# Kernel optimization log

Measured on AMD Instinct MI355X. Metric: run time of the kernel, lower is better.

## Reference

```python
import jax, jax.numpy as jnp
import numpy as np

H = 768
NHEADS = 2
MAX_REL = 96  # module's max_rel_enc; static here (positive count >> 96 for these inputs)


def _ln(x, g, b, eps=1e-5):
    m = jnp.mean(x, axis=-1, keepdims=True)
    v = jnp.var(x, axis=-1, keepdims=True)
    return (x - m) * jax.lax.rsqrt(v + eps) * g + b


def _mha(q, k, v, in_w, in_b, out_w, out_b, key_pad):
    # q [B,Lq,H], k/v [B,Lk,H], key_pad [B,Lk] bool (True = masked key)
    d = q.shape[-1]
    dh = d // NHEADS
    wq, wk, wv = jnp.split(in_w, 3, axis=0)
    bq, bk, bv = jnp.split(in_b, 3)
    qh = (q @ wq.T + bq).reshape(q.shape[0], q.shape[1], NHEADS, dh)
    kh = (k @ wk.T + bk).reshape(k.shape[0], k.shape[1], NHEADS, dh)
    vh = (v @ wv.T + bv).reshape(v.shape[0], v.shape[1], NHEADS, dh)
    scores = jnp.einsum('bqhd,bkhd->bhqk', qh, kh) / np.float32(np.sqrt(dh))
    scores = jnp.where(key_pad[:, None, None, :], jnp.float32(-1e9), scores)
    attn = jax.nn.softmax(scores, axis=-1)
    out = jnp.einsum('bhqk,bkhd->bqhd', attn, vh).reshape(q.shape)
    return out @ out_w.T + out_b


def _forward(hidden_states, logits_prev, block_mask, W_rel, b_rel,
             enc_in_w, enc_in_b, enc_out_w, enc_out_b,
             enc_l1_w, enc_l1_b, enc_l2_w, enc_l2_b,
             enc_ln1_g, enc_ln1_b, enc_ln2_g, enc_ln2_b,
             dec_in_w, dec_in_b, dec_out_w, dec_out_b,
             dec_l1_w, dec_l1_b, dec_l2_w, dec_l2_b,
             dec_ln1_g, dec_ln1_b, dec_ln2_g, dec_ln2_b,
             fc_w, fc_b):
    B, N, Hd = hidden_states.shape
    # rel_layer(cat([h_i, h_j])) == h_i @ Wa.T + h_j @ Wb.T + b  (avoids [B,N,N,2H] intermediate)
    Wa = W_rel[:, :Hd]
    Wb = W_rel[:, Hd:]
    A = hidden_states @ Wa.T   # [B,N,H]
    C = hidden_states @ Wb.T   # [B,N,H]
    feat_pair = (A[:, :, None, :] + C[:, None, :, :] + b_rel).reshape(B, N * N, Hd)

    bm = block_mask.astype(jnp.float32)
    pair_mask = (bm[:, :, None] * bm[:, None, :]).reshape(B, N * N)
    score = jax.nn.sigmoid(logits_prev).reshape(B, N * N)
    neg = (score < 0.5).astype(jnp.float32)
    neg = 1.0 - (1.0 - neg) * pair_mask           # 1 = negative-or-invalid pair
    neg = jax.lax.stop_gradient(neg)              # matches score_prev.detach_()

    # dynamic top-k gather of positive pairs (static MAX_REL here)
    idx = jnp.argsort(neg, axis=1)[:, :MAX_REL]                     # positives (neg==0) first
    enc_pad = jnp.take_along_axis(neg, idx, axis=1) > 0.5           # [B,MAX_REL]
    enc_pad = enc_pad.at[:, 0].set(False)
    feat_now = feat_pair * (1.0 - neg)[:, :, None]
    pos_pairs = jnp.take_along_axis(feat_now, idx[:, :, None], axis=1)  # [B,MAX_REL,H]

    # 1-layer transformer encoder (post-norm, ReLU, d_ff = H)
    x = pos_pairs
    x = _ln(x + _mha(x, x, x, enc_in_w, enc_in_b, enc_out_w, enc_out_b, enc_pad),
            enc_ln1_g, enc_ln1_b)
    ff = jax.nn.relu(x @ enc_l1_w.T + enc_l1_b) @ enc_l2_w.T + enc_l2_b
    patterns = _ln(x + ff, enc_ln2_g, enc_ln2_b)

    # 1-layer decoder with self_attn=False: cross-attn + FFN, post-norm
    t = feat_pair
    t = _ln(t + _mha(t, patterns, patterns, dec_in_w, dec_in_b, dec_out_w, dec_out_b, enc_pad),
            dec_ln1_g, dec_ln1_b)
    ff = jax.nn.relu(t @ dec_l1_w.T + dec_l1_b) @ dec_l2_w.T + dec_l2_b
    t = _ln(t + ff, dec_ln2_g, dec_ln2_b)

    refined = t.reshape(B, N, N, Hd)
    return (refined @ fc_w.T + fc_b)[..., 0]    # [B,N,N]


def setup_inputs() -> dict:
    key = jax.random.key(0)
    ks = jax.random.split(key, 24)
    B, N = 4, 128
    p = lambda k, s: jax.random.normal(k, s, jnp.float32) * 0.02
    return {
        'hidden_states': jax.random.normal(ks[0], (B, N, H), jnp.float32),
        'logits_prev': jax.random.normal(ks[1], (B, N, N), jnp.float32),
        'block_mask': jax.random.randint(ks[2], (B, N), 0, 2),
        'W_rel': p(ks[3], (H, 2 * H)), 'b_rel': p(ks[4], (H,)),
        'enc_in_w': p(ks[5], (3 * H, H)), 'enc_in_b': p(ks[6], (3 * H,)),
        'enc_out_w': p(ks[7], (H, H)), 'enc_out_b': p(ks[8], (H,)),
        'enc_l1_w': p(ks[9], (H, H)), 'enc_l1_b': p(ks[10], (H,)),
        'enc_l2_w': p(ks[11], (H, H)), 'enc_l2_b': p(ks[12], (H,)),
        'enc_ln1_g': jnp.ones((H,), jnp.float32), 'enc_ln1_b': jnp.zeros((H,), jnp.float32),
        'enc_ln2_g': jnp.ones((H,), jnp.float32), 'enc_ln2_b': jnp.zeros((H,), jnp.float32),
        'dec_in_w': p(ks[13], (3 * H, H)), 'dec_in_b': p(ks[14], (3 * H,)),
        'dec_out_w': p(ks[15], (H, H)), 'dec_out_b': p(ks[16], (H,)),
        'dec_l1_w': p(ks[17], (H, H)), 'dec_l1_b': p(ks[18], (H,)),
        'dec_l2_w': p(ks[19], (H, H)), 'dec_l2_b': p(ks[20], (H,)),
        'dec_ln1_g': jnp.ones((H,), jnp.float32), 'dec_ln1_b': jnp.zeros((H,), jnp.float32),
        'dec_ln2_g': jnp.ones((H,), jnp.float32), 'dec_ln2_b': jnp.zeros((H,), jnp.float32),
        'fc_w': p(ks[21], (1, H)), 'fc_b': p(ks[22], (1,)),
    }


def reference(hidden_states, logits_prev, block_mask, W_rel, b_rel,
              enc_in_w, enc_in_b, enc_out_w, enc_out_b,
              enc_l1_w, enc_l1_b, enc_l2_w, enc_l2_b,
              enc_ln1_g, enc_ln1_b, enc_ln2_g, enc_ln2_b,
              dec_in_w, dec_in_b, dec_out_w, dec_out_b,
              dec_l1_w, dec_l1_b, dec_l2_w, dec_l2_b,
              dec_ln1_g, dec_ln1_b, dec_ln2_g, dec_ln2_b,
              fc_w, fc_b):
    return _forward(hidden_states, logits_prev, block_mask, W_rel, b_rel,
                    enc_in_w, enc_in_b, enc_out_w, enc_out_b,
                    enc_l1_w, enc_l1_b, enc_l2_w, enc_l2_b,
                    enc_ln1_g, enc_ln1_b, enc_ln2_g, enc_ln2_b,
                    dec_in_w, dec_in_b, dec_out_w, dec_out_b,
                    dec_l1_w, dec_l1_b, dec_l2_w, dec_l2_b,
                    dec_ln1_g, dec_ln1_b, dec_ln2_g, dec_ln2_b,
                    fc_w, fc_b)
```

## Files before the change

### kernel.cpp

```cpp
#include <hip/hip_runtime.h>
#include <cstdint>
#include <cstddef>

typedef unsigned short u16;
typedef __attribute__((ext_vector_type(8))) short sv8;
typedef __attribute__((ext_vector_type(4))) short sv4;
typedef __attribute__((ext_vector_type(4))) float fv4;
typedef __attribute__((ext_vector_type(8))) __bf16 bv8;

#define WAITVM(N) asm volatile("s_waitcnt vmcnt(" #N ")" ::: "memory")
#define WAITLG0() asm volatile("s_waitcnt lgkmcnt(0)" ::: "memory")
#define SB0() __builtin_amdgcn_sched_barrier(0)
#define BAR() __builtin_amdgcn_s_barrier()

__device__ __forceinline__ float b2f(u16 u) {
  union { unsigned int i; float f; } v; v.i = ((unsigned int)u) << 16; return v.f;
}
__device__ __forceinline__ u16 f2b(float f) {
  union { float f; unsigned int i; } v; v.f = f;
  unsigned int r = v.i + 0x7fffu + ((v.i >> 16) & 1u);
  return (u16)(r >> 16);
}

__device__ __forceinline__ void gload16(const u16* g, u16* l) {
  __builtin_amdgcn_global_load_lds(
      (const __attribute__((address_space(1))) void*)g,
      (__attribute__((address_space(3))) void*)l, 16, 0, 0);
}

struct CvtArgs { const float* src[10]; u16* dst[10]; int n[10]; };

__global__ __launch_bounds__(256) void cvt_multi(CvtArgs a) {
  int t = blockIdx.y;
  const float* s = a.src[t];
  u16* d = a.dst[t];
  int n = a.n[t];
  int i4 = (blockIdx.x * 256 + threadIdx.x) * 4;
  if (i4 + 4 <= n) {
    float4 v = *(const float4*)(s + i4);
    sv4 o;
    o[0] = (short)f2b(v.x); o[1] = (short)f2b(v.y);
    o[2] = (short)f2b(v.z); o[3] = (short)f2b(v.w);
    *(sv4*)(d + i4) = o;
  }
}

__global__ __launch_bounds__(256) void prep_q0(
    const float* __restrict__ dec_in_w, const float* __restrict__ dec_in_b,
    const float* __restrict__ b_rel, float* __restrict__ q0) {
  int wave = threadIdx.x >> 6, lane = threadIdx.x & 63;
  int row = blockIdx.x * 4 + wave;
  const float* wrp = dec_in_w + (size_t)row * 768;
  float acc = 0.f;
  #pragma unroll
  for (int t = 0; t < 3; t++) {
    float4 wv = *(const float4*)(wrp + (t * 64 + lane) * 4);
    float4 bv = *(const float4*)(b_rel + (t * 64 + lane) * 4);
    acc += wv.x * bv.x + wv.y * bv.y + wv.z * bv.z + wv.w * bv.w;
  }
  #pragma unroll
  for (int d = 1; d <= 32; d <<= 1) acc += __shfl_xor(acc, d);
  if (lane == 0) q0[row] = acc + dec_in_b[row];
}

__global__ __launch_bounds__(256) void prep_q0k(
    const float* __restrict__ q0, const u16* __restrict__ khb,
    float* __restrict__ q0k) {
  int wave = threadIdx.x >> 6, lane = threadIdx.x & 63;
  int idx = blockIdx.x * 4 + wave;
  int b = idx / 192, c = idx % 192;
  int h = (c < 96) ? 0 : 1;
  int k = (c < 96) ? c : c - 96;
  const u16* kr = khb + ((size_t)(b * 96 + k)) * 768 + h * 384;
  const float* qp = q0 + h * 384;
  float acc = 0.f;
  #pragma unroll
  for (int t = 0; t < 6; t++) {
    int d = t * 64 + lane;
    acc += qp[d] * b2f(kr[d]);
  }
  #pragma unroll
  for (int d = 1; d <= 32; d <<= 1) acc += __shfl_xor(acc, d);
  if (lane == 0) q0k[idx] = acc * 0.05103103630798287f;
}

__global__ __launch_bounds__(256) void prep_misc(
    const float* __restrict__ dec_out_b, const float* __restrict__ b_rel,
    const float* __restrict__ ln2g, const float* __restrict__ ln2b,
    const float* __restrict__ fc_w, const float* __restrict__ fc_b,
    float* __restrict__ bb, float* __restrict__ gfc, float* __restrict__ scal) {
  int tid = threadIdx.x;
  int wave = tid >> 6, lane = tid & 63;
  float s1 = 0.f, s2 = 0.f;
  for (int t = tid; t < 768; t += 256) {
    bb[t] = dec_out_b[t] + b_rel[t];
    float gf = ln2g[t] * fc_w[t];
    gfc[t] = gf;
    s1 += gf; s2 += ln2b[t] * fc_w[t];
  }
  #pragma unroll
  for (int d = 1; d <= 32; d <<= 1) { s1 += __shfl_xor(s1, d); s2 += __shfl_xor(s2, d); }
  __shared__ float r1[4], r2[4];
  if (lane == 0) { r1[wave] = s1; r2[wave] = s2; }
  __syncthreads();
  if (tid == 0) {
    float a = r1[0] + r1[1] + r1[2] + r1[3];
    float c = r2[0] + r2[1] + r2[2] + r2[3];
    scal[1] = a;
    scal[0] = c + fc_b[0];
  }
}

__global__ __launch_bounds__(256) void select_pairs(
    const float* __restrict__ logits, const int* __restrict__ bm,
    int* __restrict__ idxb, int* __restrict__ encpad, int* __restrict__ zflag) {
  int b = blockIdx.x, tid = threadIdx.x;
  int wave = tid >> 6, lane = tid & 63;
  __shared__ unsigned char pos[16384];
  __shared__ int bml[128];
  __shared__ int wsum[4];
  const float* lg = logits + (size_t)b * 16384;
  if (tid < 128) bml[tid] = bm[b * 128 + tid];
  __syncthreads();
  for (int i = 0; i < 16; i++) {
    int e4 = (i * 256 + tid) * 4;
    float4 v = *(const float4*)(lg + e4);
    uchar4 o;
    {
      float sg = 1.f / (1.f + expf(-v.x));
      o.x = (!(sg < 0.5f)) && bml[e4 >> 7] && bml[e4 & 127];
      sg = 1.f / (1.f + expf(-v.y));
      o.y = (!(sg < 0.5f)) && bml[(e4 + 1) >> 7] && bml[(e4 + 1) & 127];
      sg = 1.f / (1.f + expf(-v.z));
      o.z = (!(sg < 0.5f)) && bml[(e4 + 2) >> 7] && bml[(e4 + 2) & 127];
      sg = 1.f / (1.f + expf(-v.w));
      o.w = (!(sg < 0.5f)) && bml[(e4 + 3) >> 7] && bml[(e4 + 3) & 127];
    }
    *(uchar4*)(pos + e4) = o;
  }
  __syncthreads();
  int cnt = 0;
  #pragma unroll 8
  for (int u = 0; u < 64; u++) cnt += pos[tid * 64 + u];
  int v = cnt;
  #pragma unroll
  for (int d = 1; d < 64; d <<= 1) { int o = __shfl_up(v, d); if (lane >= d) v += o; }
  if (lane == 63) wsum[wave] = v;
  __syncthreads();
  int wbase = 0;
  for (int w = 0; w < wave; w++) wbase += wsum[w];
  int mtot = wsum[0] + wsum[1] + wsum[2] + wsum[3];
  int pq = wbase + v - cnt;
  int nq = tid * 64 - pq;
  for (int u = 0; u < 64; u++) {
    int p = tid * 64 + u;
    if (pos[p]) {
      if (pq < 96) { idxb[b * 96 + pq] = p; encpad[b * 96 + pq] = 0; zflag[b * 96 + pq] = 0; }
      pq++;
    } else {
      int slot = mtot + nq;
      if (slot < 96) { idxb[b * 96 + slot] = p; encpad[b * 96 + slot] = 1; zflag[b * 96 + slot] = 1; }
      nq++;
    }
  }
  __syncthreads();
  if (tid == 0) encpad[b * 96] = 0;
}

__global__ __launch_bounds__(256) void gather_pp(
    const float* __restrict__ Af, const float* __restrict__ Cf,
    const float* __restrict__ b_rel, const int* __restrict__ idxb,
    const int* __restrict__ zflag, u16* __restrict__ PP) {
  int s = blockIdx.x, b = blockIdx.y;
  int slot = b * 96 + s;
  int p = idxb[slot];
  int z = zflag[slot];
  const float* ar = Af + ((size_t)b * 128 + (p >> 7)) * 768;
  const float* cr = Cf + ((size_t)b * 128 + (p & 127)) * 768;
  for (int c = threadIdx.x; c < 768; c += 256) {
    float v = z ? 0.f : (ar[c] + cr[c] + b_rel[c]);
    PP[(size_t)slot * 768 + c] = f2b(v);
  }
}

template<int EPI, int OUTM, int BM>
__global__ __launch_bounds__(256) void gemm_bt(
    const u16* __restrict__ Aptr, const u16* __restrict__ Wptr,
    const float* __restrict__ bias,
    void* __restrict__ out1, void* __restrict__ out2,
    const u16* __restrict__ resp, int ldr,
    int M, int N, int K, int lda, int ldw, int ldo,
    int ZH, int zbm, int bstr,
    long sAb, long sAh, long sWb, long sWh, long sOb, long sOh,
    float scale) {
  constexpr int FR = BM / 32;
  constexpr int BUF = BM * 32;
  int z = blockIdx.z;
  int zb = z / ZH, zh = z % ZH;
  const u16* A = Aptr + (size_t)zb * sAb + (size_t)zh * sAh;
  const u16* W = Wptr + (size_t)(zb & zbm) * sWb + (size_t)zh * sWh;
  const float* bz = bias ? bias + (size_t)zb * bstr : nullptr;
  size_t obase = (size_t)zb * sOb + (size_t)zh * sOh;

  int m0 = blockIdx.x * BM, n0 = blockIdx.y * BM;
  int tid = threadIdx.x;
  int wave = tid >> 6, lane = tid & 63;
  int wr = (wave >> 1) * (BM / 2), wc = (wave & 1) * (BM / 2);

  __shared__ __attribute__((aligned(16))) u16 As[4 * BUF];
  __shared__ __attribute__((aligned(16))) u16 Ws[4 * BUF];

  fv4 acc[FR][FR] = {};

  int srow = tid & (BM - 1);
  int scol = (BM == 128) ? ((tid >> 7) * 8) : ((tid >> 6) * 8);
  int ra = m0 + srow; if (ra > M - 1) ra = M - 1;
  int rw = n0 + srow; if (rw > N - 1) rw = N - 1;
  const u16* gA = A + (size_t)ra * lda + scol;
  const u16* gW = W + (size_t)rw * ldw + scol;
  int lofs = wave * 512;

  int rb = (lane >> 4) * (BM * 8) + (lane & 15) * 8;

  int nt = K >> 5;

  auto stage = [&](int tile) {
    int k0 = tile << 5;
    int cu = tile & 3;
    u16* la = As + cu * BUF + lofs;
    u16* lw = Ws + cu * BUF + lofs;
    gload16(gA + k0, la);
    gload16(gW + k0, lw);
    if (BM == 128) {
      gload16(gA + k0 + 16, la + 2048);
      gload16(gW + k0 + 16, lw + 2048);
    }
  };

  auto compute = [&](int cu) {
    const u16* Ap = As + cu * BUF;
    const u16* Wp = Ws + cu * BUF;
    bv8 af[FR], wf[FR];
    #pragma unroll
    for (int f = 0; f < FR; f++) af[f] = *(const bv8*)(Ap + rb + (wr + f * 16) * 8);
    #pragma unroll
    for (int f = 0; f < FR; f++) wf[f] = *(const bv8*)(Wp + rb + (wc + f * 16) * 8);
    __builtin_amdgcn_s_setprio(1);
    #pragma unroll
    for (int fm = 0; fm < FR; fm++)
      #pragma unroll
      for (int fn = 0; fn < FR; fn++)
        acc[fm][fn] = __builtin_amdgcn_mfma_f32_16x16x32_bf16(af[fm], wf[fn], acc[fm][fn], 0, 0, 0);
    __builtin_amdgcn_s_setprio(0);
  };

  stage(0); stage(1); stage(2);

  for (int t = 0; t < nt - 3; ++t) {
    if constexpr (BM == 128) WAITVM(8); else WAITVM(4);
    BAR();
    stage(t + 3);
    SB0();
    compute(t & 3);
  }
  { if constexpr (BM == 128) WAITVM(8); else WAITVM(4); BAR(); SB0(); compute((nt - 3) & 3); }
  { if constexpr (BM == 128) WAITVM(4); else WAITVM(2); BAR(); SB0(); compute((nt - 2) & 3); }
  { WAITVM(0); BAR(); SB0(); compute((nt - 1) & 3); }

  int lr4 = (lane >> 4) * 4, lc = lane & 15;
  #pragma unroll
  for (int fm = 0; fm < FR; fm++) {
    #pragma unroll
    for (int r = 0; r < 4; r++) {
      int row = m0 + wr + fm * 16 + lr4 + r;
      if (row >= M) continue;
      #pragma unroll
      for (int fn = 0; fn < FR; fn++) {
        int col = n0 + wc + fn * 16 + lc;
        if (col >= N) continue;
        float v = acc[fm][fn][r] * scale;
        if (bz) v += bz[col];
        if (EPI == 1) v = fmaxf(v, 0.f);
        if (EPI == 2) v += b2f(resp[(size_t)row * ldr + col]);
        size_t o = obase + (size_t)row * ldo + col;
        if (OUTM == 0) ((u16*)out1)[o] = f2b(v);
        else if (OUTM == 1) ((float*)out1)[o] = v;
        else { ((float*)out1)[o] = v; ((u16*)out2)[o] = f2b(v); }
      }
    }
  }
}

template<int EPI>
__global__ __launch_bounds__(512, 2) void gemm256(
    const u16* __restrict__ Aptr, const u16* __restrict__ Wptr,
    const float* __restrict__ bias, u16* __restrict__ out,
    const u16* __restrict__ resp, int ldr,
    const float* __restrict__ exA, const float* __restrict__ exC,
    int K, int lda, int ldw, int ldo,
    long zA, long zW, long zO, long zR, long zE) {
  __shared__ __attribute__((aligned(16))) u16 lds[2 * 2 * 16384];

  int nwg = gridDim.x * gridDim.y * gridDim.z;
  int lin = blockIdx.x + gridDim.x * (blockIdx.y + gridDim.y * blockIdx.z);
  int q8 = nwg >> 3;
  int swz = (lin & 7) * q8 + (lin >> 3);
  int bx = swz & 63;
  int rest = swz >> 6;
  int by = rest % 3;
  int zz = rest / 3;

  const u16* A = Aptr + (size_t)zz * zA;
  const u16* W = Wptr + (size_t)zz * zW;
  u16* outz = out + (size_t)zz * zO;
  const u16* respz = resp + (size_t)zz * zR;
  const float* exAz = exA + (size_t)zz * zE;
  const float* exCz = exC + (size_t)zz * zE;

  int m0 = bx * 256, n0 = by * 256;
  int tid = threadIdx.x;
  int wave = tid >> 6, lane = tid & 63;
  int wr = (wave >> 2) * 128;
  int wc = (wave & 3) * 64;
  int lr = lane & 15, ls = lane >> 4;
  int axor = lr & 7;

  int srow = tid >> 3;
  int schunk = (tid & 7) ^ (srow & 7);
  const u16* gA0 = A + (size_t)(m0 + srow) * lda + schunk * 8;
  const u16* gW0 = W + (size_t)(n0 + srow) * ldw + schunk * 8;
  int wofs = wave * 512;

  fv4 acc[8][4] = {};

  auto stageA = [&](int t, int q) {
    gload16(gA0 + (size_t)q * 64 * lda + t * 64,
            lds + (t & 1) * 32768 + q * 4096 + wofs);
  };
  auto stageW = [&](int t, int q) {
    gload16(gW0 + (size_t)q * 64 * ldw + t * 64,
            lds + (t & 1) * 32768 + 16384 + q * 4096 + wofs);
  };

  int TH = K >> 6;
  #pragma unroll
  for (int q = 0; q < 4; q++) stageA(0, q);
  #pragma unroll
  for (int q = 0; q < 4; q++) stageW(0, q);
  WAITVM(0);
  BAR();

  for (int t = 0; t < TH; ++t) {
    const u16* Ab = lds + (t & 1) * 32768;
    const u16* Wb = Ab + 16384;
    bool st = (t + 1 < TH);
    bv8 af[4], wf[4];
    #pragma unroll
    for (int n = 0; n < 4; n++)
      wf[n] = *(const bv8*)(Wb + (wc + n * 16 + lr) * 64 + (ls ^ axor) * 8);
    #pragma unroll
    for (int f = 0; f < 4; f++)
      af[f] = *(const bv8*)(Ab + (wr + f * 16 + lr) * 64 + (ls ^ axor) * 8);
    if (st) { stageA(t + 1, 0); stageA(t + 1, 1); }
    WAITLG0(); SB0();
    __builtin_amdgcn_s_setprio(1);
    #pragma unroll
    for (int f = 0; f < 4; f++)
      #pragma unroll
      for (int n = 0; n < 4; n++)
        acc[f][n] = __builtin_amdgcn_mfma_f32_16x16x32_bf16(af[f], wf[n], acc[f][n], 0, 0, 0);
    __builtin_amdgcn_s_setprio(0);
    #pragma unroll
    for (int f = 0; f < 4; f++)
      af[f] = *(const bv8*)(Ab + (wr + 64 + f * 16 + lr) * 64 + (ls ^ axor) * 8);
    if (st) { stageA(t + 1, 2); stageA(t + 1, 3); stageW(t + 1, 0); }
    WAITLG0(); SB0();
    __builtin_amdgcn_s_setprio(1);
    #pragma unroll
    for (int f = 0; f < 4; f++)
      #pragma unroll
      for (int n = 0; n < 4; n++)
        acc[4 + f][n] = __builtin_amdgcn_mfma_f32_16x16x32_bf16(af[f], wf[n], acc[4 + f][n], 0, 0, 0);
    __builtin_amdgcn_s_setprio(0);
    #pragma unroll
    for (int n = 0; n < 4; n++)
      wf[n] = *(const bv8*)(Wb + (wc + n * 16 + lr) * 64 + ((ls + 4) ^ axor) * 8);
    #pragma unroll
    for (int f = 0; f < 4; f++)
      af[f] = *(const bv8*)(Ab + (wr + f * 16 + lr) * 64 + ((ls + 4) ^ axor) * 8);
    if (st) { stageW(t + 1, 1); stageW(t + 1, 2); stageW(t + 1, 3); }
    WAITLG0(); SB0();
    __builtin_amdgcn_s_setprio(1);
    #pragma unroll
    for (int f = 0; f < 4; f++)
      #pragma unroll
      for (int n = 0; n < 4; n++)
        acc[f][n] = __builtin_amdgcn_mfma_f32_16x16x32_bf16(af[f], wf[n], acc[f][n], 0, 0, 0);
    __builtin_amdgcn_s_setprio(0);
    #pragma unroll
    for (int f = 0; f < 4; f++)
      af[f] = *(const bv8*)(Ab + (wr + 64 + f * 16 + lr) * 64 + ((ls + 4) ^ axor) * 8);
    WAITLG0(); SB0();
    __builtin_amdgcn_s_setprio(1);
    #pragma unroll
    for (int f = 0; f < 4; f++)
      #pragma unroll
      for (int n = 0; n < 4; n++)
        acc[4 + f][n] = __builtin_amdgcn_mfma_f32_16x16x32_bf16(af[f], wf[n], acc[4 + f][n], 0, 0, 0);
    __builtin_amdgcn_s_setprio(0);
    if (st) WAITVM(0);
    BAR();
  }

  int lr4 = (lane >> 4) * 4, lc = lane & 15;
  #pragma unroll
  for (int fm = 0; fm < 8; fm++) {
    #pragma unroll
    for (int r = 0; r < 4; r++) {
      int row = m0 + wr + (fm >> 2) * 64 + (fm & 3) * 16 + lr4 + r;
      #pragma unroll
      for (int fn = 0; fn < 4; fn++) {
        int col = n0 + wc + fn * 16 + lc;
        float v = acc[fm][fn][r] + bias[col];
        if (EPI == 1) v = fmaxf(v, 0.f);
        if (EPI == 2) v += b2f(respz[(size_t)row * ldr + col]);
        if (EPI == 3) v += exAz[(size_t)(row >> 7) * 768 + col] + exCz[(size_t)(row & 127) * 768 + col];
        outz[(size_t)row * ldo + col] = f2b(v);
      }
    }
  }
}

__global__ __launch_bounds__(128) void enc_att(
    const u16* __restrict__ QKV, const int* __restrict__ encpad, u16* __restrict__ AO) {
  int s = blockIdx.x;
  int bh = blockIdx.y;
  int b = bh >> 1, h = bh & 1;
  int tid = threadIdx.x;
  __shared__ float q[384];
  __shared__ float sc[96];
  __shared__ float red[2];
  size_t rowq = ((size_t)b * 96 + s) * 2304;
  for (int d = tid; d < 384; d += 128) q[d] = b2f(QKV[rowq + h * 384 + d]);
  __syncthreads();
  if (tid < 96) {
    const u16* kr = QKV + ((size_t)b * 96 + tid) * 2304 + 768 + h * 384;
    float acc = 0.f;
    for (int d = 0; d < 384; d++) acc += q[d] * b2f(kr[d]);
    acc *= 0.05103103630798287f;
    if (encpad[b * 96 + tid]) acc = -1e9f;
    sc[tid] = acc;
  }
  __syncthreads();
  if (tid == 0) {
    float m = sc[0];
    for (int k = 1; k < 96; k++) m = fmaxf(m, sc[k]);
    red[0] = m;
  }
  __syncthreads();
  if (tid < 96) sc[tid] = __expf(sc[tid] - red[0]);
  __syncthreads();
  if (tid == 0) {
    float sum = 0.f;
    for (int k = 0; k < 96; k++) sum += sc[k];
    red[1] = 1.f / sum;
  }
  __syncthreads();
  float inv = red[1];
  for (int d = tid; d < 384; d += 128) {
    const u16* vb = QKV + (size_t)b * 96 * 2304 + 1536 + h * 384 + d;
    float acc = 0.f;
    for (int k = 0; k < 96; k++) acc += sc[k] * b2f(vb[(size_t)k * 2304]);
    AO[((size_t)b * 96 + s) * 768 + h * 384 + d] = f2b(acc * inv);
  }
}

__global__ __launch_bounds__(256) void softmax_pairs(
    const float* __restrict__ SA, const float* __restrict__ SC,
    const float* __restrict__ q0k,
    const int* __restrict__ encpad, u16* __restrict__ P) {
  int wave = threadIdx.x >> 6, lane = threadIdx.x & 63;
  int bi = blockIdx.y;
  int p = blockIdx.x * 4 + wave;
  int i = p >> 7, j = p & 127;
  const float* sa = SA + ((size_t)bi * 128 + i) * 192;
  const float* sc = SC + ((size_t)bi * 128 + j) * 192;
  const float* qk = q0k + bi * 192;
  int c0 = lane * 3;
  float s0, s1, s2;
  {
    int c = c0;     int k = (c < 96) ? c : c - 96;
    s0 = encpad[bi * 96 + k] ? -1e9f : (sa[c] + sc[c] + qk[c]);
    c = c0 + 1;     k = (c < 96) ? c : c - 96;
    s1 = encpad[bi * 96 + k] ? -1e9f : (sa[c] + sc[c] + qk[c]);
    c = c0 + 2;     k = (c < 96) ? c : c - 96;
    s2 = encpad[bi * 96 + k] ? -1e9f : (sa[c] + sc[c] + qk[c]);
  }
  float m = fmaxf(s0, fmaxf(s1, s2));
  #pragma unroll
  for (int d = 1; d <= 16; d <<= 1) m = fmaxf(m, __shfl_xor(m, d));
  float e0 = __expf(s0 - m), e1 = __expf(s1 - m), e2 = __expf(s2 - m);
  float sum = e0 + e1 + e2;
  #pragma unroll
  for (int d = 1; d <= 16; d <<= 1) sum += __shfl_xor(sum, d);
  float inv = 1.f / sum;
  u16* o = P + ((size_t)bi * 16384 + p) * 192 + c0;
  o[0] = f2b(e0 * inv); o[1] = f2b(e1 * inv); o[2] = f2b(e2 * inv);
}

__global__ __launch_bounds__(256) void ln_rows(
    const u16* __restrict__ Y, const float* __restrict__ g,
    const float* __restrict__ bt, u16* __restrict__ X, int rows) {
  int wave = threadIdx.x >> 6, lane = threadIdx.x & 63;
  int row = blockIdx.x * 4 + wave;
  if (row >= rows) return;
  const u16* y = Y + (size_t)row * 768;
  sv8 v1 = *(const sv8*)(y + lane * 8);
  sv4 v2 = *(const sv4*)(y + 512 + lane * 4);
  float x[12];
  #pragma unroll
  for (int t = 0; t < 8; t++) x[t] = b2f((u16)v1[t]);
  #pragma unroll
  for (int t = 0; t < 4; t++) x[8 + t] = b2f((u16)v2[t]);
  float s = 0.f, q = 0.f;
  #pragma unroll
  for (int t = 0; t < 12; t++) { s += x[t]; q += x[t] * x[t]; }
  #pragma unroll
  for (int d = 1; d <= 32; d <<= 1) { s += __shfl_xor(s, d); q += __shfl_xor(q, d); }
  float mean = s * (1.f / 768.f);
  float var = q * (1.f / 768.f) - mean * mean;
  float rstd = rsqrtf(var + 1e-5f);
  u16* xo = X + (size_t)row * 768;
  sv8 w1; sv4 w2;
  #pragma unroll
  for (int t = 0; t < 8; t++) {
    int c = lane * 8 + t;
    w1[t] = (short)f2b((x[t] - mean) * rstd * g[c] + bt[c]);
  }
  #pragma unroll
  for (int t = 0; t < 4; t++) {
    int c = 512 + lane * 4 + t;
    w2[t] = (short)f2b((x[8 + t] - mean) * rstd * g[c] + bt[c]);
  }
  *(sv8*)(xo + lane * 8) = w1;
  *(sv4*)(xo + 512 + lane * 4) = w2;
}

__global__ __launch_bounds__(256) void final_rows(
    const u16* __restrict__ Y, const float* __restrict__ gfc,
    const float* __restrict__ scal, float* __restrict__ out, int rows) {
  int wave = threadIdx.x >> 6, lane = threadIdx.x & 63;
  int row = blockIdx.x * 4 + wave;
  if (row >= rows) return;
  const u16* y = Y + (size_t)row * 768;
  sv8 v1 = *(const sv8*)(y + lane * 8);
  sv4 v2 = *(const sv4*)(y + 512 + lane * 4);
  float x[12];
  #pragma unroll
  for (int t = 0; t < 8; t++) x[t] = b2f((u16)v1[t]);
  #pragma unroll
  for (int t = 0; t < 4; t++) x[8 + t] = b2f((u16)v2[t]);
  float s = 0.f, q = 0.f, sg = 0.f;
  #pragma unroll
  for (int t = 0; t < 8; t++) {
    int c = lane * 8 + t;
    s += x[t]; q += x[t] * x[t]; sg += x[t] * gfc[c];
  }
  #pragma unroll
  for (int t = 0; t < 4; t++) {
    int c = 512 + lane * 4 + t;
    s += x[8 + t]; q += x[8 + t] * x[8 + t]; sg += x[8 + t] * gfc[c];
  }
  #pragma unroll
  for (int d = 1; d <= 32; d <<= 1) {
    s += __shfl_xor(s, d); q += __shfl_xor(q, d); sg += __shfl_xor(sg, d);
  }
  float mean = s * (1.f / 768.f);
  float var = q * (1.f / 768.f) - mean * mean;
  float rstd = rsqrtf(var + 1e-5f);
  if (lane == 0) out[row] = rstd * (sg - mean * scal[1]) + scal[0];
}

extern "C" void kernel_launch(void* const* d_in, const int* in_sizes, int n_in,
                              void* d_out, int out_size, void* d_ws, size_t ws_size,
                              hipStream_t stream) {
  (void)in_sizes; (void)n_in; (void)out_size;
  const float* hs        = (const float*)d_in[0];
  const float* logits    = (const float*)d_in[1];
  const int*   bmask     = (const int*)d_in[2];
  const float* W_rel     = (const float*)d_in[3];
  const float* b_rel     = (const float*)d_in[4];
  const float* enc_in_w  = (const float*)d_in[5];
  const float* enc_in_b  = (const float*)d_in[6];
  const float* enc_out_w = (const float*)d_in[7];
  const float* enc_out_b = (const float*)d_in[8];
  const float* enc_l1_w  = (const float*)d_in[9];
  const float* enc_l1_b  = (const float*)d_in[10];
  const float* enc_l2_w  = (const float*)d_in[11];
  const float* enc_l2_b  = (const float*)d_in[12];
  const float* enc_ln1_g = (const float*)d_in[13];
  const float* enc_ln1_b = (const float*)d_in[14];
  const float* enc_ln2_g = (const float*)d_in[15];
  const float* enc_ln2_b = (const float*)d_in[16];
  const float* dec_in_w  = (const float*)d_in[17];
  const float* dec_in_b  = (const float*)d_in[18];
  const float* dec_out_w = (const float*)d_in[19];
  const float* dec_out_b = (const float*)d_in[20];
  const float* dec_l1_w  = (const float*)d_in[21];
  const float* dec_l1_b  = (const float*)d_in[22];
  const float* dec_l2_w  = (const float*)d_in[23];
  const float* dec_l2_b  = (const float*)d_in[24];
  const float* dec_ln1_g = (const float*)d_in[25];
  const float* dec_ln1_b = (const float*)d_in[26];
  const float* dec_ln2_g = (const float*)d_in[27];
  const float* dec_ln2_b = (const float*)d_in[28];
  const float* fc_w      = (const float*)d_in[29];
  const float* fc_b      = (const float*)d_in[30];

  char* base = (char*)d_ws;
  size_t off = 0;
  auto alloc = [&](size_t bytes) -> void* {
    size_t o = (off + 255) & ~(size_t)255;
    off = o + bytes;
    return (void*)(base + o);
  };

  u16* hsb   = (u16*)alloc((size_t)393216 * 2);
  u16* wrelb = (u16*)alloc((size_t)1179648 * 2);
  u16* eiwb  = (u16*)alloc((size_t)1769472 * 2);
  u16* eowb  = (u16*)alloc((size_t)589824 * 2);
  u16* el1b  = (u16*)alloc((size_t)589824 * 2);
  u16* el2b  = (u16*)alloc((size_t)589824 * 2);
  u16* diwb  = (u16*)alloc((size_t)1769472 * 2);
  u16* dowb  = (u16*)alloc((size_t)589824 * 2);
  u16* dl1b  = (u16*)alloc((size_t)589824 * 2);
  u16* dl2b  = (u16*)alloc((size_t)589824 * 2);
  float* Af  = (float*)alloc((size_t)786432 * 4);
  float* Cf  = Af + 393216;
  u16* ACb   = (u16*)alloc((size_t)786432 * 2);
  float* q0  = (float*)alloc(768 * 4);
  float* q0k = (float*)alloc(768 * 4);
  float* bbv = (float*)alloc(768 * 4);
  float* gfc = (float*)alloc(768 * 4);
  float* scal = (float*)alloc(4 * 4);
  int* idxb   = (int*)alloc(384 * 4);
  int* encpadb = (int*)alloc(384 * 4);
  int* zflagb  = (int*)alloc(384 * 4);
  u16* PPb   = (u16*)alloc((size_t)294912 * 2);
  u16* QKVe  = (u16*)alloc((size_t)884736 * 2);
  u16* AOe   = (u16*)alloc((size_t)294912 * 2);
  u16* Ye    = (u16*)alloc((size_t)294912 * 2);
  u16* Xe    = (u16*)alloc((size_t)294912 * 2);
  u16* He    = (u16*)alloc((size_t)294912 * 2);
  u16* Y2e   = (u16*)alloc((size_t)294912 * 2);
  u16* patternsb = (u16*)alloc((size_t)294912 * 2);
  u16* khb   = (u16*)alloc((size_t)294912 * 2);
  u16* vhb   = (u16*)alloc((size_t)294912 * 2);
  u16* AqCqb = (u16*)alloc((size_t)786432 * 2);
  float* SASCf = (float*)alloc((size_t)196608 * 4);
  u16* VOTb  = (u16*)alloc((size_t)589824 * 2);
  u16* Pb    = (u16*)alloc((size_t)12582912 * 2);

  const size_t ACT1 = (size_t)12582912 * 2;
  size_t fixed = (off + 255) & ~(size_t)255;
  int NB = 1;
  if (fixed + 2 * 4 * ACT1 + 4096 <= ws_size) NB = 4;
  else if (fixed + 2 * 2 * ACT1 + 4096 <= ws_size) NB = 2;
  u16* Y1buf = (u16*)alloc((size_t)NB * 12582912 * 2);
  u16* H1buf = (u16*)alloc((size_t)NB * 12582912 * 2);

  CvtArgs ca{};
  int ci = 0;
  auto addc = [&](const float* s, u16* d, int n) { ca.src[ci] = s; ca.dst[ci] = d; ca.n[ci] = n; ci++; };
  addc(hs, hsb, 393216);        addc(W_rel, wrelb, 1179648);
  addc(enc_in_w, eiwb, 1769472); addc(enc_out_w, eowb, 589824);
  addc(enc_l1_w, el1b, 589824);  addc(enc_l2_w, el2b, 589824);
  addc(dec_in_w, diwb, 1769472); addc(dec_out_w, dowb, 589824);
  addc(dec_l1_w, dl1b, 589824);  addc(dec_l2_w, dl2b, 589824);
  cvt_multi<<<dim3(1728, 10, 1), 256, 0, stream>>>(ca);

  prep_q0<<<192, 256, 0, stream>>>(dec_in_w, dec_in_b, b_rel, q0);
  prep_misc<<<1, 256, 0, stream>>>(dec_out_b, b_rel, dec_ln2_g, dec_ln2_b, fc_w, fc_b,
                                   bbv, gfc, scal);
  select_pairs<<<dim3(4, 1, 1), 256, 0, stream>>>(logits, bmask, idxb, encpadb, zflagb);

  gemm_bt<0, 2, 64><<<dim3(8, 12, 2), 256, 0, stream>>>(hsb, wrelb, nullptr, Af, ACb,
      nullptr, 0, 512, 768, 768, 768, 1536, 768,
      1, -1, 0, 0, 0, 768, 0, 393216, 0, 1.f);

  gather_pp<<<dim3(96, 4, 1), 256, 0, stream>>>(Af, Cf, b_rel, idxb, zflagb, PPb);

  gemm_bt<0, 0, 64><<<dim3(6, 36, 1), 256, 0, stream>>>(PPb, eiwb, enc_in_b, QKVe, nullptr,
      nullptr, 0, 384, 2304, 768, 768, 768, 2304,
      1, -1, 0, 0, 0, 0, 0, 0, 0, 1.f);
  enc_att<<<dim3(96, 8, 1), 128, 0, stream>>>(QKVe, encpadb, AOe);
  gemm_bt<2, 0, 64><<<dim3(6, 12, 1), 256, 0, stream>>>(AOe, eowb, enc_out_b, Ye, nullptr,
      PPb, 768, 384, 768, 768, 768, 768, 768,
      1, -1, 0, 0, 0, 0, 0, 0, 0, 1.f);
  ln_rows<<<96, 256, 0, stream>>>(Ye, enc_ln1_g, enc_ln1_b, Xe, 384);
  gemm_bt<1, 0, 64><<<dim3(6, 12, 1), 256, 0, stream>>>(Xe, el1b, enc_l1_b, He, nullptr,
      nullptr, 0, 384, 768, 768, 768, 768, 768,
      1, -1, 0, 0, 0, 0, 0, 0, 0, 1.f);
  gemm_bt<2, 0, 64><<<dim3(6, 12, 1), 256, 0, stream>>>(He, el2b, enc_l2_b, Y2e, nullptr,
      Xe, 768, 384, 768, 768, 768, 768, 768,
      1, -1, 0, 0, 0, 0, 0, 0, 0, 1.f);
  ln_rows<<<96, 256, 0, stream>>>(Y2e, enc_ln2_g, enc_ln2_b, patternsb, 384);

  gemm_bt<0, 0, 64><<<dim3(6, 12, 2), 256, 0, stream>>>(patternsb, diwb + (size_t)768 * 768,
      dec_in_b + 768, khb, nullptr, nullptr, 0,
      384, 768, 768, 768, 768, 768,
      1, -1, 768, 0, 0, 589824, 0, 294912, 0, 1.f);
  prep_q0k<<<192, 256, 0, stream>>>(q0, khb, q0k);
  gemm_bt<0, 0, 64><<<dim3(16, 12, 1), 256, 0, stream>>>(ACb, diwb, nullptr, AqCqb, nullptr,
      nullptr, 0, 1024, 768, 768, 768, 768, 768,
      1, -1, 0, 0, 0, 0, 0, 0, 0, 1.f);
  const float scl = 0.05103103630798287f;
  gemm_bt<0, 1, 64><<<dim3(2, 2, 16), 256, 0, stream>>>(AqCqb, khb, nullptr, SASCf, nullptr,
      nullptr, 0, 128, 96, 384, 768, 768, 192,
      2, 3, 0, 98304, 384, 73728, 384, 24576, 96, scl);
  gemm_bt<0, 0, 64><<<dim3(12, 2, 8), 256, 0, stream>>>(dowb, vhb, nullptr, VOTb, nullptr,
      nullptr, 0, 768, 96, 384, 768, 768, 192,
      2, -1, 0, 0, 384, 73728, 384, 147456, 96, 1.f);

  softmax_pairs<<<dim3(4096, 4), 256, 0, stream>>>(SASCf, SASCf + 98304, q0k, encpadb, Pb);
  const long PB_B = 3145728, VOT_B = 147456, ACT_B = 12582912, EX_B = 98304;
  for (int g = 0; g < 4; g += NB) {
    gemm256<3><<<dim3(64, 3, NB), 512, 0, stream>>>(
        Pb + (size_t)g * PB_B, VOTb + (size_t)g * VOT_B, bbv, Y1buf,
        Y1buf, 0, Af + (size_t)g * EX_B, Cf + (size_t)g * EX_B,
        192, 192, 192, 768, PB_B, VOT_B, ACT_B, 0, EX_B);
    ln_rows<<<NB * 4096, 256, 0, stream>>>(Y1buf, dec_ln1_g, dec_ln1_b, Y1buf, NB * 16384);
    gemm256<1><<<dim3(64, 3, NB), 512, 0, stream>>>(
        Y1buf, dl1b, dec_l1_b, H1buf, H1buf, 0, Af, Cf,
        768, 768, 768, 768, ACT_B, 0, ACT_B, 0, 0);
    gemm256<2><<<dim3(64, 3, NB), 512, 0, stream>>>(
        H1buf, dl2b, dec_l2_b, Y1buf, Y1buf, 768, Af, Cf,
        768, 768, 768, 768, ACT_B, 0, ACT_B, ACT_B, 0);
    final_rows<<<NB * 4096, 256, 0, stream>>>(Y1buf, gfc, scal,
        (float*)d_out + (size_t)g * 16384, NB * 16384);
  }
}
```

Measured before the change: 522.5 us.

## Stage pair-feature addends in LDS and remap gemm256 tiles for XCD locality

The EPI==3 epilogue no longer reads fp32 A/C pair-feature addends from global memory per element. It now stages bf16 copies of them (from the ACb buffer) into the reused LDS tile buffer and reads them from there. The workgroup-to-tile mapping is also rewritten so consecutive tiles on each XCD share the same M rows across N-columns and batch slices, which is meant to improve L2 reuse. Switching from fp32 to bf16 addends changes the precision of the added terms slightly, and the new mapping hardcodes a 64x3 grid.

```diff
diff --git a/kernel.cpp b/kernel.cpp
--- a/kernel.cpp
+++ b/kernel.cpp
@@ -296,26 +296,27 @@
     const u16* __restrict__ Aptr, const u16* __restrict__ Wptr,
     const float* __restrict__ bias, u16* __restrict__ out,
     const u16* __restrict__ resp, int ldr,
-    const float* __restrict__ exA, const float* __restrict__ exC,
+    const u16* __restrict__ exA, const u16* __restrict__ exC,
     int K, int lda, int ldw, int ldo,
     long zA, long zW, long zO, long zR, long zE) {
   __shared__ __attribute__((aligned(16))) u16 lds[2 * 2 * 16384];
 
-  int nwg = gridDim.x * gridDim.y * gridDim.z;
-  int lin = blockIdx.x + gridDim.x * (blockIdx.y + gridDim.y * blockIdx.z);
-  int q8 = nwg >> 3;
-  int swz = (lin & 7) * q8 + (lin >> 3);
-  int bx = swz & 63;
-  int rest = swz >> 6;
-  int by = rest % 3;
-  int zz = rest / 3;
+  int nzz = gridDim.z;
+  int lin = blockIdx.x + 64 * (blockIdx.y + 3 * blockIdx.z);
+  int xcd = lin & 7;
+  int s = lin >> 3;
+  int grp = s / (3 * nzz);
+  int rem = s - grp * (3 * nzz);
+  int by = rem / nzz;
+  int zz = rem - by * nzz;
+  int bx = xcd + 8 * grp;
 
   const u16* A = Aptr + (size_t)zz * zA;
   const u16* W = Wptr + (size_t)zz * zW;
   u16* outz = out + (size_t)zz * zO;
   const u16* respz = resp + (size_t)zz * zR;
-  const float* exAz = exA + (size_t)zz * zE;
-  const float* exCz = exC + (size_t)zz * zE;
+  const u16* exAz = exA + (size_t)zz * zE;
+  const u16* exCz = exC + (size_t)zz * zE;
 
   int m0 = bx * 256, n0 = by * 256;
   int tid = threadIdx.x;
@@ -412,6 +413,20 @@
     BAR();
   }
 
+  if (EPI == 3) {
+    for (int c = tid; c < 4096; c += 512) {
+      int rrow = c >> 5, c8 = c & 31;
+      *(sv8*)(lds + (size_t)c * 8) =
+          *(const sv8*)(exCz + (size_t)rrow * 768 + n0 + c8 * 8);
+    }
+    if (tid < 64) {
+      int rrow = tid >> 5, c8 = tid & 31;
+      *(sv8*)(lds + 32768 + (size_t)tid * 8) =
+          *(const sv8*)(exAz + (size_t)(bx * 2 + rrow) * 768 + n0 + c8 * 8);
+    }
+    __syncthreads();
+  }
+
   int lr4 = (lane >> 4) * 4, lc = lane & 15;
   #pragma unroll
   for (int fm = 0; fm < 8; fm++) {
@@ -424,7 +439,8 @@
         float v = acc[fm][fn][r] + bias[col];
         if (EPI == 1) v = fmaxf(v, 0.f);
         if (EPI == 2) v += b2f(respz[(size_t)row * ldr + col]);
-        if (EPI == 3) v += exAz[(size_t)(row >> 7) * 768 + col] + exCz[(size_t)(row & 127) * 768 + col];
+        if (EPI == 3) v += b2f(lds[32768 + (size_t)((row - m0) >> 7) * 256 + (col - n0)])
+                         + b2f(lds[(size_t)(row & 127) * 256 + (col - n0)]);
         outz[(size_t)row * ldo + col] = f2b(v);
       }
     }
@@ -723,18 +739,21 @@
       2, -1, 0, 0, 384, 73728, 384, 147456, 96, 1.f);
 
   softmax_pairs<<<dim3(4096, 4), 256, 0, stream>>>(SASCf, SASCf + 98304, q0k, encpadb, Pb);
-  const long PB_B = 3145728, VOT_B = 147456, ACT_B = 12582912, EX_B = 98304;
+  const long PB_B = 3145728, VOT_B = 147456, ACT_B = 12582912;
+  const long EXU_B = 98304;
   for (int g = 0; g < 4; g += NB) {
     gemm256<3><<<dim3(64, 3, NB), 512, 0, stream>>>(
         Pb + (size_t)g * PB_B, VOTb + (size_t)g * VOT_B, bbv, Y1buf,
-        Y1buf, 0, Af + (size_t)g * EX_B, Cf + (size_t)g * EX_B,
-        192, 192, 192, 768, PB_B, VOT_B, ACT_B, 0, EX_B);
+        Y1buf, 0,
+        ACb + (size_t)g * EXU_B,
+        ACb + 393216 + (size_t)g * EXU_B,
+        192, 192, 192, 768, PB_B, VOT_B, ACT_B, 0, EXU_B);
     ln_rows<<<NB * 4096, 256, 0, stream>>>(Y1buf, dec_ln1_g, dec_ln1_b, Y1buf, NB * 16384);
     gemm256<1><<<dim3(64, 3, NB), 512, 0, stream>>>(
-        Y1buf, dl1b, dec_l1_b, H1buf, H1buf, 0, Af, Cf,
+        Y1buf, dl1b, dec_l1_b, H1buf, H1buf, 0, ACb, ACb,
         768, 768, 768, 768, ACT_B, 0, ACT_B, 0, 0);
     gemm256<2><<<dim3(64, 3, NB), 512, 0, stream>>>(
-        H1buf, dl2b, dec_l2_b, Y1buf, Y1buf, 768, Af, Cf,
+        H1buf, dl2b, dec_l2_b, Y1buf, Y1buf, 768, ACb, ACb,
         768, 768, 768, 768, ACT_B, 0, ACT_B, ACT_B, 0);
     final_rows<<<NB * 4096, 256, 0, stream>>>(Y1buf, gfc, scal,
         (float*)d_out + (size_t)g * 16384, NB * 16384);
```

After: 507.0 us. 1.03x faster.
